# Kernel optimization log

Measured on AMD Instinct MI355X. Metric: run time of the kernel, lower is better.

## Reference

```python
import jax, jax.numpy as jnp
import numpy as np
from jax import lax

B, T, V, E, H, O = 32, 64, 30000, 64, 64, 7


def setup_inputs() -> dict:
    key = jax.random.key(0)
    ks = jax.random.split(key, 17)
    s_in = 1.0 / np.sqrt(E)
    s_h = 1.0 / np.sqrt(H)
    inp = {
        "x": jax.random.uniform(ks[0], (B, T, V), dtype=jnp.float32),
        "vocab_embed": 0.02 * jax.random.normal(ks[1], (V, E), dtype=jnp.float32),
        "W_ir": s_in * jax.random.normal(ks[2], (H, E), dtype=jnp.float32),
        "W_iz": s_in * jax.random.normal(ks[3], (H, E), dtype=jnp.float32),
        "W_in": s_in * jax.random.normal(ks[4], (H, E), dtype=jnp.float32),
        "W_hr": s_h * jax.random.normal(ks[5], (H, H), dtype=jnp.float32),
        "W_hz": s_h * jax.random.normal(ks[6], (H, H), dtype=jnp.float32),
        "W_hn": s_h * jax.random.normal(ks[7], (H, H), dtype=jnp.float32),
        "b_ir": s_h * jax.random.normal(ks[8], (H,), dtype=jnp.float32),
        "b_iz": s_h * jax.random.normal(ks[9], (H,), dtype=jnp.float32),
        "b_in": s_h * jax.random.normal(ks[10], (H,), dtype=jnp.float32),
        "b_hr": s_h * jax.random.normal(ks[11], (H,), dtype=jnp.float32),
        "b_hz": s_h * jax.random.normal(ks[12], (H,), dtype=jnp.float32),
        "b_hn": s_h * jax.random.normal(ks[13], (H,), dtype=jnp.float32),
        "W_out": s_h * jax.random.normal(ks[14], (O, H), dtype=jnp.float32),
        "b_out": s_h * jax.random.normal(ks[15], (O,), dtype=jnp.float32),
        "prediction_point": T,
    }
    return inp


def reference(x, vocab_embed, W_ir, W_iz, W_in, W_hr, W_hz, W_hn,
              b_ir, b_iz, b_in, b_hr, b_hz, b_hn, W_out, b_out,
              prediction_point):
    # embed_x = relu((x @ vocab_embed) / x.sum(-1, keepdims))  -> [B, T, E]
    embed_x = jax.nn.relu(jnp.einsum("btv,ve->bte", x, vocab_embed)
                          / jnp.sum(x, axis=2, keepdims=True))

    # t = 0: no hidden contribution at all (faithful to original)
    e0 = embed_x[:, 0, :]
    z1 = jax.nn.sigmoid(e0 @ W_iz.T + b_iz)
    n1 = jnp.tanh(e0 @ W_in.T + b_in)
    h0 = (1.0 - z1) * n1  # [B, H]

    def step(h, e_t):
        hr = h @ W_hr.T + b_hr
        r = jax.nn.sigmoid(e_t @ W_ir.T + b_ir + hr)
        z = jax.nn.sigmoid(e_t @ W_iz.T + b_iz + h @ W_hz.T + b_hz)
        # NOTE: original code uses hidden_reset (W_hr) here, not hidden_new
        n = jnp.tanh(e_t @ W_in.T + b_in + r * hr)
        h_new = (1.0 - z) * n + z * h
        return h_new, None

    # scan over t = 1 .. prediction_point-1
    es = jnp.swapaxes(embed_x[:, 1:prediction_point, :], 0, 1)  # [T-1, B, E]
    h_final, _ = lax.scan(step, h0, es)

    return h_final @ W_out.T + b_out  # [B, O] logits (prob=False)
```

## Files before the change

kernel.cpp:

```cpp
#include <hip/hip_runtime.h>
#include <hip/hip_bf16.h>

typedef unsigned short u16;
typedef short short8 __attribute__((ext_vector_type(8)));
typedef float floatx4 __attribute__((ext_vector_type(4)));

#define BB 32
#define TT 64
#define VV 30000
#define EE 64
#define HH 64
#define OO 7
#define KSPLIT 32
#define NU32 937

__device__ __forceinline__ u16 f2b(float f) {
    unsigned u = __float_as_uint(f);
    u += 0x7FFFu + ((u >> 16) & 1u);
    return (u16)(u >> 16);
}

__device__ __forceinline__ unsigned pk2(float fo, float fe) {
    return __builtin_amdgcn_perm(__float_as_uint(fo), __float_as_uint(fe), 0x07060302u);
}

__device__ __forceinline__ float sigmoid_f(float x) {
    return 1.f / (1.f + __expf(-x));
}

__device__ __forceinline__ float tanh_f(float x) {
    float a = fabsf(x);
    float e = __expf(-2.f * a);
    float t = (1.f - e) / (1.f + e);
    return x < 0.f ? -t : t;
}

__global__ __launch_bounds__(256) void kT(const float* __restrict__ VE, u16* __restrict__ VTf) {
    __shared__ u16 tile[64][72];
    int v0 = blockIdx.x * 64;
    int t = threadIdx.x;
    #pragma unroll
    for (int it = 0; it < 4; ++it) {
        int c = it * 256 + t;
        int row = c >> 4, col4 = (c & 15) * 4;
        ushort4 s; s.x = 0; s.y = 0; s.z = 0; s.w = 0;
        if (v0 + row < VV) {
            float4 d = *(const float4*)(VE + (size_t)(v0 + row) * EE + col4);
            s.x = f2b(d.x); s.y = f2b(d.y); s.z = f2b(d.z); s.w = f2b(d.w);
        }
        *(ushort4*)&tile[row][col4] = s;
    }
    __syncthreads();
    int e = t & 63;
    int nb = e >> 4, r = e & 15;
    #pragma unroll
    for (int half = 0; half < 2; ++half) {
        int q8 = (t >> 6) + half * 4;
        int u = (v0 >> 5) + (q8 >> 2);
        int kin = (q8 & 3) * 8;
        u16 tmp[8];
        #pragma unroll
        for (int jj = 0; jj < 8; ++jj) tmp[jj] = tile[q8 * 8 + jj][e];
        *(uint4*)&VTf[(size_t)u * 2048 + nb * 512 + r * 32 + kin] = *(uint4*)tmp;
    }
}

__global__ __launch_bounds__(256) void kE(const float* __restrict__ x, const u16* __restrict__ vtf,
                                          float* __restrict__ Cpart, float* __restrict__ Rpart) {
    int tid = threadIdx.x;
    int w = tid >> 6, l = tid & 63;
    int r15 = l & 15, q = l >> 4;
    int mb = blockIdx.x, kb = blockIdx.y;
    int m0 = mb * 64;
    int wr = m0 + w * 16;
    int u0 = (kb * NU32) / KSPLIT, u1 = ((kb + 1) * NU32) / KSPLIT;

    const float* aP = x + (size_t)(wr + r15) * VV + u0 * 32 + q * 8;
    const u16*   bP = vtf + (size_t)u0 * 2048 + r15 * 32 + q * 8;

    floatx4 acc[4] = {};
    floatx4 accS = {};
    short8 ones;
    #pragma unroll
    for (int i = 0; i < 8; ++i) ones[i] = (short)0x3F80;

    #pragma unroll 4
    for (int u = u0; u < u1; ++u) {
        float4 a0 = *(const float4*)(aP);
        float4 a1 = *(const float4*)(aP + 4);
        short8 bf0 = *(const short8*)(bP);
        short8 bf1 = *(const short8*)(bP + 512);
        short8 bf2 = *(const short8*)(bP + 1024);
        short8 bf3 = *(const short8*)(bP + 1536);
        short8 af;
        unsigned* afu = (unsigned*)&af;
        afu[0] = pk2(a0.y, a0.x);
        afu[1] = pk2(a0.w, a0.z);
        afu[2] = pk2(a1.y, a1.x);
        afu[3] = pk2(a1.w, a1.z);
        acc[0] = __builtin_amdgcn_mfma_f32_16x16x32_bf16(af, bf0, acc[0], 0, 0, 0);
        acc[1] = __builtin_amdgcn_mfma_f32_16x16x32_bf16(af, bf1, acc[1], 0, 0, 0);
        acc[2] = __builtin_amdgcn_mfma_f32_16x16x32_bf16(af, bf2, acc[2], 0, 0, 0);
        acc[3] = __builtin_amdgcn_mfma_f32_16x16x32_bf16(af, bf3, acc[3], 0, 0, 0);
        accS   = __builtin_amdgcn_mfma_f32_16x16x32_bf16(af, ones, accS, 0, 0, 0);
        aP += 32;
        bP += 2048;
    }

    if (kb == KSPLIT - 1) {
        short8 af;
        #pragma unroll
        for (int i = 0; i < 8; ++i) af[i] = 0;
        if (q < 2) {
            float4 a0 = *(const float4*)(aP);
            float4 a1 = *(const float4*)(aP + 4);
            unsigned* afu = (unsigned*)&af;
            afu[0] = pk2(a0.y, a0.x);
            afu[1] = pk2(a0.w, a0.z);
            afu[2] = pk2(a1.y, a1.x);
            afu[3] = pk2(a1.w, a1.z);
        }
        short8 bf0 = *(const short8*)(bP);
        short8 bf1 = *(const short8*)(bP + 512);
        short8 bf2 = *(const short8*)(bP + 1024);
        short8 bf3 = *(const short8*)(bP + 1536);
        acc[0] = __builtin_amdgcn_mfma_f32_16x16x32_bf16(af, bf0, acc[0], 0, 0, 0);
        acc[1] = __builtin_amdgcn_mfma_f32_16x16x32_bf16(af, bf1, acc[1], 0, 0, 0);
        acc[2] = __builtin_amdgcn_mfma_f32_16x16x32_bf16(af, bf2, acc[2], 0, 0, 0);
        acc[3] = __builtin_amdgcn_mfma_f32_16x16x32_bf16(af, bf3, acc[3], 0, 0, 0);
        accS   = __builtin_amdgcn_mfma_f32_16x16x32_bf16(af, ones, accS, 0, 0, 0);
    }

    float* Cp = Cpart + (size_t)kb * (2048 * 64);
    #pragma unroll
    for (int r = 0; r < 4; ++r) {
        int row = wr + q * 4 + r;
        #pragma unroll
        for (int n = 0; n < 4; ++n)
            Cp[(size_t)row * 64 + n * 16 + r15] = acc[n][r];
        if (r15 == 0) Rpart[kb * 2048 + row] = accS[r];
    }
}

__global__ __launch_bounds__(256) void kGS(const float* __restrict__ Cpart, const float* __restrict__ Rpart,
                                           const float* __restrict__ Wir, const float* __restrict__ Wiz,
                                           const float* __restrict__ Win,
                                           const float* __restrict__ bir, const float* __restrict__ biz,
                                           const float* __restrict__ bin,
                                           const float* __restrict__ Whr, const float* __restrict__ Whz,
                                           const float* __restrict__ bhr, const float* __restrict__ bhz,
                                           const float* __restrict__ Wout, const float* __restrict__ bout,
                                           float* __restrict__ out) {
    __shared__ __align__(16) u16 eL[64 * 72];
    __shared__ float rsinv[64];
    __shared__ float Xs[3][64][64];
    __shared__ float hsh[64];
    int tid = threadIdx.x;
    int b = blockIdx.x;
    int m0 = b * 64;

    if (tid < 64) {
        float rs = 0.f;
        #pragma unroll
        for (int kb = 0; kb < KSPLIT; ++kb)
            rs += Rpart[kb * 2048 + m0 + tid];
        rsinv[tid] = 1.f / rs;
    }
    float4 a4[4];
    #pragma unroll
    for (int r = 0; r < 4; ++r) { a4[r].x = 0.f; a4[r].y = 0.f; a4[r].z = 0.f; a4[r].w = 0.f; }
    const float* cp = Cpart + (size_t)m0 * 64 + tid * 4;
    #pragma unroll 4
    for (int kb = 0; kb < KSPLIT; ++kb) {
        #pragma unroll
        for (int r = 0; r < 4; ++r) {
            float4 v = *(const float4*)(cp + (size_t)kb * (2048 * 64) + r * 1024);
            a4[r].x += v.x; a4[r].y += v.y; a4[r].z += v.z; a4[r].w += v.w;
        }
    }
    __syncthreads();
    #pragma unroll
    for (int r = 0; r < 4; ++r) {
        int m = r * 16 + (tid >> 4);
        float ri = rsinv[m];
        float e0 = a4[r].x * ri, e1 = a4[r].y * ri, e2 = a4[r].z * ri, e3 = a4[r].w * ri;
        e0 = e0 > 0.f ? e0 : 0.f;  e1 = e1 > 0.f ? e1 : 0.f;
        e2 = e2 > 0.f ? e2 : 0.f;  e3 = e3 > 0.f ? e3 : 0.f;
        ushort4 s;
        s.x = f2b(e0); s.y = f2b(e1); s.z = f2b(e2); s.w = f2b(e3);
        *(ushort4*)&eL[m * 72 + (tid & 15) * 4] = s;
    }
    __syncthreads();

    int w = tid >> 6, l = tid & 63;
    int r15 = l & 15, q = l >> 4;
    short8 fa0 = *(const short8*)&eL[(w * 16 + r15) * 72 + q * 8];
    short8 fa1 = *(const short8*)&eL[(w * 16 + r15) * 72 + 32 + q * 8];

    floatx4 acc[3][4] = {};
    #pragma unroll
    for (int g = 0; g < 3; ++g) {
        const float* W = (g == 0) ? Wir : (g == 1) ? Wiz : Win;
        #pragma unroll
        for (int nb = 0; nb < 4; ++nb) {
            const float* wrow = W + (nb * 16 + r15) * 64 + q * 8;
            float4 w0 = *(const float4*)(wrow);
            float4 w1 = *(const float4*)(wrow + 4);
            float4 w2 = *(const float4*)(wrow + 32);
            float4 w3 = *(const float4*)(wrow + 36);
            short8 b0, b1;
            unsigned* b0u = (unsigned*)&b0; unsigned* b1u = (unsigned*)&b1;
            b0u[0] = pk2(w0.y, w0.x); b0u[1] = pk2(w0.w, w0.z);
            b0u[2] = pk2(w1.y, w1.x); b0u[3] = pk2(w1.w, w1.z);
            b1u[0] = pk2(w2.y, w2.x); b1u[1] = pk2(w2.w, w2.z);
            b1u[2] = pk2(w3.y, w3.x); b1u[3] = pk2(w3.w, w3.z);
            acc[g][nb] = __builtin_amdgcn_mfma_f32_16x16x32_bf16(fa0, b0, acc[g][nb], 0, 0, 0);
            acc[g][nb] = __builtin_amdgcn_mfma_f32_16x16x32_bf16(fa1, b1, acc[g][nb], 0, 0, 0);
        }
    }

    #pragma unroll
    for (int g = 0; g < 3; ++g) {
        const float* bo = (g == 0) ? bir : (g == 1) ? biz : bin;
        #pragma unroll
        for (int nb = 0; nb < 4; ++nb) {
            int j = nb * 16 + r15;
            float bias = bo[j];
            #pragma unroll
            for (int r = 0; r < 4; ++r) {
                int t = w * 16 + q * 4 + r;
                Xs[g][t][j] = acc[g][nb][r] + bias;
            }
        }
    }
    if (w == 0 && q == 0) {
        #pragma unroll
        for (int nb = 0; nb < 4; ++nb) {
            int j = nb * 16 + r15;
            float z1 = sigmoid_f(acc[1][nb][0] + biz[j]);
            float n1 = tanh_f(acc[2][nb][0] + bin[j]);
            hsh[j] = (1.f - z1) * n1;
        }
    }
    __syncthreads();

    if (tid >= 64) return;
    int i = tid;
    float wrg[64], wzg[64];
    #pragma unroll
    for (int c = 0; c < 16; ++c) {
        float4 v1 = *(const float4*)(Whr + i * 64 + c * 4);
        float4 v2 = *(const float4*)(Whz + i * 64 + c * 4);
        wrg[c * 4 + 0] = v1.x; wrg[c * 4 + 1] = v1.y; wrg[c * 4 + 2] = v1.z; wrg[c * 4 + 3] = v1.w;
        wzg[c * 4 + 0] = v2.x; wzg[c * 4 + 1] = v2.y; wzg[c * 4 + 2] = v2.z; wzg[c * 4 + 3] = v2.w;
    }
    float h = hsh[i];
    float bri = bhr[i], bzi = bhz[i];

    for (int t = 1; t < 64; ++t) {
        float xr = Xs[0][t][i], xz = Xs[1][t][i], xn = Xs[2][t][i];
        float p0 = 0.f, p1 = 0.f, p2 = 0.f, p3 = 0.f;
        float z0 = 0.f, z1 = 0.f, z2 = 0.f, z3 = 0.f;
        unsigned hu = __float_as_uint(h);
        #pragma unroll
        for (int j = 0; j < 64; j += 4) {
            float h0 = __uint_as_float(__builtin_amdgcn_readlane(hu, j + 0));
            float h1 = __uint_as_float(__builtin_amdgcn_readlane(hu, j + 1));
            float h2 = __uint_as_float(__builtin_amdgcn_readlane(hu, j + 2));
            float h3 = __uint_as_float(__builtin_amdgcn_readlane(hu, j + 3));
            p0 += h0 * wrg[j + 0]; p1 += h1 * wrg[j + 1];
            p2 += h2 * wrg[j + 2]; p3 += h3 * wrg[j + 3];
            z0 += h0 * wzg[j + 0]; z1 += h1 * wzg[j + 1];
            z2 += h2 * wzg[j + 2]; z3 += h3 * wzg[j + 3];
        }
        float hr = bri + ((p0 + p1) + (p2 + p3));
        float hz = bzi + ((z0 + z1) + (z2 + z3));
        float r = sigmoid_f(xr + hr);
        float z = sigmoid_f(xz + hz);
        float n = tanh_f(xn + r * hr);
        h = (1.f - z) * n + z * h;
    }

    hsh[i] = h;
    if (i < OO) {
        float a = bout[i];
        #pragma unroll 8
        for (int j = 0; j < 64; ++j)
            a += hsh[j] * Wout[i * 64 + j];
        out[b * OO + i] = a;
    }
}

extern "C" void kernel_launch(void* const* d_in, const int* in_sizes, int n_in,
                              void* d_out, int out_size, void* d_ws, size_t ws_size,
                              hipStream_t stream) {
    const float* x    = (const float*)d_in[0];
    const float* VE   = (const float*)d_in[1];
    const float* Wir  = (const float*)d_in[2];
    const float* Wiz  = (const float*)d_in[3];
    const float* Win  = (const float*)d_in[4];
    const float* Whr  = (const float*)d_in[5];
    const float* Whz  = (const float*)d_in[6];
    const float* bir  = (const float*)d_in[8];
    const float* biz  = (const float*)d_in[9];
    const float* bin  = (const float*)d_in[10];
    const float* bhr  = (const float*)d_in[11];
    const float* bhz  = (const float*)d_in[12];
    const float* Wout = (const float*)d_in[14];
    const float* bout = (const float*)d_in[15];

    char* ws = (char*)d_ws;
    u16*   VTf   = (u16*)(ws);
    float* Cpart = (float*)(ws + 4000000);
    float* Rpart = (float*)(ws + 20777216);

    kT<<<469, 256, 0, stream>>>(VE, VTf);
    kE<<<dim3(2048 / 64, KSPLIT), 256, 0, stream>>>(x, VTf, Cpart, Rpart);
    kGS<<<BB, 256, 0, stream>>>(Cpart, Rpart, Wir, Wiz, Win, bir, biz, bin,
                                Whr, Whz, bhr, bhz, Wout, bout, (float*)d_out);
}
```

Measured before the change: 422.8 us.

## Split fused reduce/GRU kernel into parallel reduction kernel and sequential scan kernel

The former single kernel did the split-K reduction, input projection and GRU recurrence in 32 blocks. Now a 128-block kernel reduces the partial sums, normalises, and computes the three input-gate projections, writing them to a workspace buffer. A separate 64-thread-per-block kernel then loads that buffer into shared memory and runs the recurrence, broadcasting h through LDS instead of readlane and using packed float2 FMAs. The goal is to spread the memory-bound Cpart reduction across more CUs and shorten the serial scan, at the cost of an extra launch and a global round trip for the projections.

Result: no change. 419.2 us (-0.9%).

```diff
diff --git a/kernel.cpp b/kernel.cpp
--- a/kernel.cpp
+++ b/kernel.cpp
@@ -4,6 +4,7 @@
 typedef unsigned short u16;
 typedef short short8 __attribute__((ext_vector_type(8)));
 typedef float floatx4 __attribute__((ext_vector_type(4)));
+typedef float float2v __attribute__((ext_vector_type(2)));
 
 #define BB 32
 #define TT 64
@@ -142,151 +143,145 @@
     }
 }
 
-__global__ __launch_bounds__(256) void kGS(const float* __restrict__ Cpart, const float* __restrict__ Rpart,
-                                           const float* __restrict__ Wir, const float* __restrict__ Wiz,
-                                           const float* __restrict__ Win,
-                                           const float* __restrict__ bir, const float* __restrict__ biz,
-                                           const float* __restrict__ bin,
-                                           const float* __restrict__ Whr, const float* __restrict__ Whz,
-                                           const float* __restrict__ bhr, const float* __restrict__ bhz,
-                                           const float* __restrict__ Wout, const float* __restrict__ bout,
-                                           float* __restrict__ out) {
-    __shared__ __align__(16) u16 eL[64 * 72];
-    __shared__ float rsinv[64];
-    __shared__ float Xs[3][64][64];
-    __shared__ float hsh[64];
+__global__ __launch_bounds__(256) void kR(const float* __restrict__ Cpart, const float* __restrict__ Rpart,
+                                          const float* __restrict__ Wir, const float* __restrict__ Wiz,
+                                          const float* __restrict__ Win,
+                                          const float* __restrict__ bir, const float* __restrict__ biz,
+                                          const float* __restrict__ bin,
+                                          float* __restrict__ X) {
+    __shared__ float rsinv[16];
+    __shared__ u16 eL[16 * 72];
     int tid = threadIdx.x;
-    int b = blockIdx.x;
-    int m0 = b * 64;
-
-    if (tid < 64) {
+    int m0 = blockIdx.x * 16;
+
+    if (tid < 16) {
         float rs = 0.f;
         #pragma unroll
         for (int kb = 0; kb < KSPLIT; ++kb)
             rs += Rpart[kb * 2048 + m0 + tid];
         rsinv[tid] = 1.f / rs;
     }
-    float4 a4[4];
-    #pragma unroll
-    for (int r = 0; r < 4; ++r) { a4[r].x = 0.f; a4[r].y = 0.f; a4[r].z = 0.f; a4[r].w = 0.f; }
+
+    float4 a; a.x = 0.f; a.y = 0.f; a.z = 0.f; a.w = 0.f;
     const float* cp = Cpart + (size_t)m0 * 64 + tid * 4;
-    #pragma unroll 4
+    #pragma unroll 8
     for (int kb = 0; kb < KSPLIT; ++kb) {
-        #pragma unroll
-        for (int r = 0; r < 4; ++r) {
-            float4 v = *(const float4*)(cp + (size_t)kb * (2048 * 64) + r * 1024);
-            a4[r].x += v.x; a4[r].y += v.y; a4[r].z += v.z; a4[r].w += v.w;
-        }
+        float4 v = *(const float4*)(cp + (size_t)kb * (2048 * 64));
+        a.x += v.x; a.y += v.y; a.z += v.z; a.w += v.w;
     }
     __syncthreads();
-    #pragma unroll
-    for (int r = 0; r < 4; ++r) {
-        int m = r * 16 + (tid >> 4);
-        float ri = rsinv[m];
-        float e0 = a4[r].x * ri, e1 = a4[r].y * ri, e2 = a4[r].z * ri, e3 = a4[r].w * ri;
+    {
+        int row = tid >> 4;
+        float ri = rsinv[row];
+        float e0 = a.x * ri, e1 = a.y * ri, e2 = a.z * ri, e3 = a.w * ri;
         e0 = e0 > 0.f ? e0 : 0.f;  e1 = e1 > 0.f ? e1 : 0.f;
         e2 = e2 > 0.f ? e2 : 0.f;  e3 = e3 > 0.f ? e3 : 0.f;
         ushort4 s;
         s.x = f2b(e0); s.y = f2b(e1); s.z = f2b(e2); s.w = f2b(e3);
-        *(ushort4*)&eL[m * 72 + (tid & 15) * 4] = s;
+        *(ushort4*)&eL[row * 72 + (tid & 15) * 4] = s;
     }
     __syncthreads();
 
     int w = tid >> 6, l = tid & 63;
     int r15 = l & 15, q = l >> 4;
-    short8 fa0 = *(const short8*)&eL[(w * 16 + r15) * 72 + q * 8];
-    short8 fa1 = *(const short8*)&eL[(w * 16 + r15) * 72 + 32 + q * 8];
-
-    floatx4 acc[3][4] = {};
+    short8 fa0 = *(const short8*)&eL[r15 * 72 + q * 8];
+    short8 fa1 = *(const short8*)&eL[r15 * 72 + 32 + q * 8];
+
+    #pragma unroll
+    for (int un = 0; un < 3; ++un) {
+        int u = w * 3 + un;
+        int g = u >> 2, nb = u & 3;
+        const float* W  = (g == 0) ? Wir : (g == 1) ? Wiz : Win;
+        const float* bo = (g == 0) ? bir : (g == 1) ? biz : bin;
+        const float* wrow = W + (nb * 16 + r15) * 64 + q * 8;
+        float4 w0 = *(const float4*)(wrow);
+        float4 w1 = *(const float4*)(wrow + 4);
+        float4 w2 = *(const float4*)(wrow + 32);
+        float4 w3 = *(const float4*)(wrow + 36);
+        short8 b0, b1;
+        unsigned* b0u = (unsigned*)&b0; unsigned* b1u = (unsigned*)&b1;
+        b0u[0] = pk2(w0.y, w0.x); b0u[1] = pk2(w0.w, w0.z);
+        b0u[2] = pk2(w1.y, w1.x); b0u[3] = pk2(w1.w, w1.z);
+        b1u[0] = pk2(w2.y, w2.x); b1u[1] = pk2(w2.w, w2.z);
+        b1u[2] = pk2(w3.y, w3.x); b1u[3] = pk2(w3.w, w3.z);
+        floatx4 acc = {};
+        acc = __builtin_amdgcn_mfma_f32_16x16x32_bf16(fa0, b0, acc, 0, 0, 0);
+        acc = __builtin_amdgcn_mfma_f32_16x16x32_bf16(fa1, b1, acc, 0, 0, 0);
+        float bias = bo[nb * 16 + r15];
+        #pragma unroll
+        for (int r = 0; r < 4; ++r) {
+            int row = q * 4 + r;
+            X[((size_t)g * 2048 + m0 + row) * 64 + nb * 16 + r15] = acc[r] + bias;
+        }
+    }
+}
+
+__global__ __launch_bounds__(64) void kS(const float* __restrict__ X,
+                                         const float* __restrict__ Whr, const float* __restrict__ Whz,
+                                         const float* __restrict__ bhr, const float* __restrict__ bhz,
+                                         const float* __restrict__ Wout, const float* __restrict__ bout,
+                                         float* __restrict__ out) {
+    __shared__ __align__(16) float Xs[3][64][64];
+    __shared__ __align__(16) float hbc[64];
+    int i = threadIdx.x;
+    int b = blockIdx.x;
+
+    const float* src = X + (size_t)b * 64 * 64;
     #pragma unroll
     for (int g = 0; g < 3; ++g) {
-        const float* W = (g == 0) ? Wir : (g == 1) ? Wiz : Win;
-        #pragma unroll
-        for (int nb = 0; nb < 4; ++nb) {
-            const float* wrow = W + (nb * 16 + r15) * 64 + q * 8;
-            float4 w0 = *(const float4*)(wrow);
-            float4 w1 = *(const float4*)(wrow + 4);
-            float4 w2 = *(const float4*)(wrow + 32);
-            float4 w3 = *(const float4*)(wrow + 36);
-            short8 b0, b1;
-            unsigned* b0u = (unsigned*)&b0; unsigned* b1u = (unsigned*)&b1;
-            b0u[0] = pk2(w0.y, w0.x); b0u[1] = pk2(w0.w, w0.z);
-            b0u[2] = pk2(w1.y, w1.x); b0u[3] = pk2(w1.w, w1.z);
-            b1u[0] = pk2(w2.y, w2.x); b1u[1] = pk2(w2.w, w2.z);
-            b1u[2] = pk2(w3.y, w3.x); b1u[3] = pk2(w3.w, w3.z);
-            acc[g][nb] = __builtin_amdgcn_mfma_f32_16x16x32_bf16(fa0, b0, acc[g][nb], 0, 0, 0);
-            acc[g][nb] = __builtin_amdgcn_mfma_f32_16x16x32_bf16(fa1, b1, acc[g][nb], 0, 0, 0);
-        }
-    }
-
-    #pragma unroll
-    for (int g = 0; g < 3; ++g) {
-        const float* bo = (g == 0) ? bir : (g == 1) ? biz : bin;
-        #pragma unroll
-        for (int nb = 0; nb < 4; ++nb) {
-            int j = nb * 16 + r15;
-            float bias = bo[j];
-            #pragma unroll
-            for (int r = 0; r < 4; ++r) {
-                int t = w * 16 + q * 4 + r;
-                Xs[g][t][j] = acc[g][nb][r] + bias;
-            }
-        }
-    }
-    if (w == 0 && q == 0) {
-        #pragma unroll
-        for (int nb = 0; nb < 4; ++nb) {
-            int j = nb * 16 + r15;
-            float z1 = sigmoid_f(acc[1][nb][0] + biz[j]);
-            float n1 = tanh_f(acc[2][nb][0] + bin[j]);
-            hsh[j] = (1.f - z1) * n1;
-        }
-    }
-    __syncthreads();
-
-    if (tid >= 64) return;
-    int i = tid;
-    float wrg[64], wzg[64];
+        const float4* s4 = (const float4*)(src + (size_t)g * 2048 * 64);
+        float4* d4 = (float4*)&Xs[g][0][0];
+        #pragma unroll
+        for (int c = 0; c < 16; ++c)
+            d4[c * 64 + i] = s4[c * 64 + i];
+    }
+
+    float2v wr2[32], wz2[32];
     #pragma unroll
     for (int c = 0; c < 16; ++c) {
         float4 v1 = *(const float4*)(Whr + i * 64 + c * 4);
         float4 v2 = *(const float4*)(Whz + i * 64 + c * 4);
-        wrg[c * 4 + 0] = v1.x; wrg[c * 4 + 1] = v1.y; wrg[c * 4 + 2] = v1.z; wrg[c * 4 + 3] = v1.w;
-        wzg[c * 4 + 0] = v2.x; wzg[c * 4 + 1] = v2.y; wzg[c * 4 + 2] = v2.z; wzg[c * 4 + 3] = v2.w;
-    }
-    float h = hsh[i];
+        float2v a01 = {v1.x, v1.y}, a23 = {v1.z, v1.w};
+        float2v b01 = {v2.x, v2.y}, b23 = {v2.z, v2.w};
+        wr2[c * 2] = a01; wr2[c * 2 + 1] = a23;
+        wz2[c * 2] = b01; wz2[c * 2 + 1] = b23;
+    }
     float bri = bhr[i], bzi = bhz[i];
+    __syncthreads();
+
+    float h;
+    {
+        float z1 = sigmoid_f(Xs[1][0][i]);
+        float n1 = tanh_f(Xs[2][0][i]);
+        h = (1.f - z1) * n1;
+    }
 
     for (int t = 1; t < 64; ++t) {
+        hbc[i] = h;
         float xr = Xs[0][t][i], xz = Xs[1][t][i], xn = Xs[2][t][i];
-        float p0 = 0.f, p1 = 0.f, p2 = 0.f, p3 = 0.f;
-        float z0 = 0.f, z1 = 0.f, z2 = 0.f, z3 = 0.f;
-        unsigned hu = __float_as_uint(h);
+        float2v ar0 = {0.f, 0.f}, ar1 = {0.f, 0.f};
+        float2v az0 = {0.f, 0.f}, az1 = {0.f, 0.f};
         #pragma unroll
         for (int j = 0; j < 64; j += 4) {
-            float h0 = __uint_as_float(__builtin_amdgcn_readlane(hu, j + 0));
-            float h1 = __uint_as_float(__builtin_amdgcn_readlane(hu, j + 1));
-            float h2 = __uint_as_float(__builtin_amdgcn_readlane(hu, j + 2));
-            float h3 = __uint_as_float(__builtin_amdgcn_readlane(hu, j + 3));
-            p0 += h0 * wrg[j + 0]; p1 += h1 * wrg[j + 1];
-            p2 += h2 * wrg[j + 2]; p3 += h3 * wrg[j + 3];
-            z0 += h0 * wzg[j + 0]; z1 += h1 * wzg[j + 1];
-            z2 += h2 * wzg[j + 2]; z3 += h3 * wzg[j + 3];
+            float4 hv = *(const float4*)&hbc[j];
+            float2v hA = {hv.x, hv.y}, hB = {hv.z, hv.w};
+            ar0 += hA * wr2[j >> 1]; ar1 += hB * wr2[(j >> 1) + 1];
+            az0 += hA * wz2[j >> 1]; az1 += hB * wz2[(j >> 1) + 1];
         }
-        float hr = bri + ((p0 + p1) + (p2 + p3));
-        float hz = bzi + ((z0 + z1) + (z2 + z3));
+        float hr = bri + ((ar0.x + ar0.y) + (ar1.x + ar1.y));
+        float hz = bzi + ((az0.x + az0.y) + (az1.x + az1.y));
         float r = sigmoid_f(xr + hr);
         float z = sigmoid_f(xz + hz);
         float n = tanh_f(xn + r * hr);
         h = (1.f - z) * n + z * h;
     }
 
-    hsh[i] = h;
+    hbc[i] = h;
     if (i < OO) {
         float a = bout[i];
         #pragma unroll 8
         for (int j = 0; j < 64; ++j)
-            a += hsh[j] * Wout[i * 64 + j];
+            a += hbc[j] * Wout[i * 64 + j];
         out[b * OO + i] = a;
     }
 }
@@ -313,9 +308,10 @@
     u16*   VTf   = (u16*)(ws);
     float* Cpart = (float*)(ws + 4000000);
     float* Rpart = (float*)(ws + 20777216);
+    float* Xg    = (float*)(ws + 21039360);
 
     kT<<<469, 256, 0, stream>>>(VE, VTf);
     kE<<<dim3(2048 / 64, KSPLIT), 256, 0, stream>>>(x, VTf, Cpart, Rpart);
-    kGS<<<BB, 256, 0, stream>>>(Cpart, Rpart, Wir, Wiz, Win, bir, biz, bin,
-                                Whr, Whz, bhr, bhz, Wout, bout, (float*)d_out);
-}
+    kR<<<128, 256, 0, stream>>>(Cpart, Rpart, Wir, Wiz, Win, bir, biz, bin, Xg);
+    kS<<<BB, 64, 0, stream>>>(Xg, Whr, Whz, bhr, bhz, Wout, bout, (float*)d_out);
+}
```
